# Optimization experiments

Measured on AMD Instinct MI355X. Metric: run time of the kernel, lower is better.

## Reference

```python
import jax, jax.numpy as jnp
import numpy as np

VOCAB = 50257
EMBED = 1024

def setup_inputs() -> dict:
    key = jax.random.key(0)
    k1, k2 = jax.random.split(key)
    hidden_states = jax.random.normal(k1, (2, 2048, EMBED), dtype=jnp.float32)
    # nn.Linear weight: [vocab_size, embed_dim], no bias
    W = jax.random.normal(k2, (VOCAB, EMBED), dtype=jnp.float32) * (1.0 / np.sqrt(EMBED))
    return {"hidden_states": hidden_states, "W": W}

def reference(hidden_states, W):
    # logits: [B, S, V] = hidden @ W^T
    logits = jnp.einsum("bsd,vd->bsv", hidden_states, W)
    return jax.nn.log_softmax(logits, axis=-1)
```

## Files before the change

### kernel.cpp

```cpp
#include <hip/hip_runtime.h>
#include <hip/hip_bf16.h>
#include <math.h>

#define VOCAB 50257
#define VPAD  50432
#define EMB   1024
#define NROWS 4096

#define BM 256
#define BN 256
#define BK 64
#define NKT (EMB / BK)
#define NMT (NROWS / BM)
#define NT  (VPAD / BN)
#define NWG (NMT * NT)

typedef __attribute__((ext_vector_type(4))) float  f32x4;
typedef __attribute__((ext_vector_type(4), aligned(4))) float f32x4u;
typedef __attribute__((ext_vector_type(4))) __bf16 bf16x4;
typedef __attribute__((ext_vector_type(8))) __bf16 bf16x8;

#define FENCE asm volatile("" ::: "memory")
#define BARRIER do { FENCE; __builtin_amdgcn_s_barrier(); FENCE; } while (0)

__global__ __launch_bounds__(256)
void cvt_bf16(const float* __restrict__ src, __bf16* __restrict__ dst,
              long n_src, long n_dst) {
    long i = ((long)blockIdx.x * 256 + threadIdx.x) * 8;
    if (i >= n_dst) return;
    bf16x8 o;
    if (i < n_src) {
        f32x4 a = *(const f32x4*)(src + i);
        f32x4 b = *(const f32x4*)(src + i + 4);
        #pragma unroll
        for (int e = 0; e < 4; ++e) {
            o[e]     = (__bf16)a[e];
            o[4 + e] = (__bf16)b[e];
        }
    } else {
        #pragma unroll
        for (int e = 0; e < 8; ++e) o[e] = (__bf16)0.0f;
    }
    *(bf16x8*)(dst + i) = o;
}

template <bool LB_OUT>
__global__ __launch_bounds__(512, 2)
void gemm_fused(const __bf16* __restrict__ A, const __bf16* __restrict__ B,
                float* __restrict__ C, __bf16* __restrict__ Lb,
                float* __restrict__ pbuf) {
    __shared__ alignas(16) __bf16 S[65536];

    const int tid  = threadIdx.x;
    const int lane = tid & 63;
    const int wave = tid >> 6;
    const int wm   = (wave >> 2) * 128;
    const int wn   = (wave & 3) * 64;
    const int frow = lane & 15;
    const int hi   = lane >> 4;

    const int b  = blockIdx.x;
    const int lg = (b & 7) * (NWG / 8) + (b >> 3);
    const int mt = lg & (NMT - 1);
    const int nt = lg >> 4;
    const int mtB = mt * BM, ntB = nt * BN;

    const int r0 = tid >> 3;
    const int ls = (tid & 7) ^ (r0 & 7);
    const __bf16* gA = A + (size_t)(mtB + r0) * EMB + ls * 8;
    const __bf16* gB = B + (size_t)(ntB + r0) * EMB + ls * 8;

    f32x4 acc[8][4];
    const f32x4 vzero = {0.f, 0.f, 0.f, 0.f};
    #pragma unroll
    for (int m = 0; m < 8; ++m)
        #pragma unroll
        for (int n = 0; n < 4; ++n) acc[m][n] = vzero;

#define STAGE_UNIT(bc, kt, u) do {                                            \
        const __bf16* g_ = ((u) < 2 ? gB : gA) + ((size_t)(((u)&1) * 128) * EMB + (kt) * BK); \
        __bf16* d_ = &S[(bc) * 32768 + ((u) < 2 ? 16384 : 0) + ((u)&1) * 8192 + wave * 512]; \
        __builtin_amdgcn_global_load_lds(                                     \
            (const __attribute__((address_space(1))) void*)g_,               \
            (__attribute__((address_space(3))) void*)d_, 16, 0, 0);          \
        __builtin_amdgcn_global_load_lds(                                     \
            (const __attribute__((address_space(1))) void*)(g_ + (size_t)64 * EMB), \
            (__attribute__((address_space(3))) void*)(d_ + 4096), 16, 0, 0); \
    } while (0)

#define LDA_F(c, mh, ks) { _Pragma("unroll")                                  \
    for (int i_ = 0; i_ < 4; ++i_) {                                          \
        const int row_ = wm + ((mh) * 4 + i_) * 16 + frow;                    \
        af[i_] = *(const bf16x8*)&S[(c) * 32768 + row_ * 64 + ((((ks) * 4 + hi)) ^ (row_ & 7)) * 8]; } }

#define LDB_F(c, ks) { _Pragma("unroll")                                      \
    for (int n_ = 0; n_ < 4; ++n_) {                                          \
        const int row_ = wn + n_ * 16 + frow;                                 \
        bfr[n_] = *(const bf16x8*)&S[(c) * 32768 + 16384 + row_ * 64 + ((((ks) * 4 + hi)) ^ (row_ & 7)) * 8]; } }

#define MFMA16(mh)                                                            \
    __builtin_amdgcn_s_setprio(1);                                            \
    _Pragma("unroll") for (int i_ = 0; i_ < 4; ++i_)                          \
        _Pragma("unroll") for (int n_ = 0; n_ < 4; ++n_)                      \
            acc[(mh) * 4 + i_][n_] = __builtin_amdgcn_mfma_f32_16x16x32_bf16( \
                af[i_], bfr[n_], acc[(mh) * 4 + i_][n_], 0, 0, 0);            \
    __builtin_amdgcn_s_setprio(0);

    bf16x8 af[4], bfr[4];

    #pragma unroll
    for (int u = 0; u < 4; ++u) STAGE_UNIT(0, 0, u);

    int cur = 0;
    for (int t = 0; t < NKT; ++t) {
        const int c = cur;
        const bool pf = (t + 1 < NKT);
        if (pf) {
            STAGE_UNIT(c ^ 1, t + 1, 0);
            asm volatile("s_waitcnt vmcnt(2)" ::: "memory");
        } else {
            asm volatile("s_waitcnt vmcnt(0)" ::: "memory");
        }
        BARRIER;
        LDB_F(c, 0); LDA_F(c, 0, 0); MFMA16(0);
        if (pf) STAGE_UNIT(c ^ 1, t + 1, 1);
        LDA_F(c, 1, 0); MFMA16(1);
        if (pf) STAGE_UNIT(c ^ 1, t + 1, 2);
        LDB_F(c, 1); LDA_F(c, 0, 1); MFMA16(0);
        if (pf) STAGE_UNIT(c ^ 1, t + 1, 3);
        LDA_F(c, 1, 1); MFMA16(1);
        BARRIER;
        cur ^= 1;
    }
#undef STAGE_UNIT

    __syncthreads();
    const bool edge = (ntB + BN > VOCAB);

    if (LB_OUT) {
        #pragma unroll
        for (int m = 0; m < 8; ++m) {
            const size_t rbase = (size_t)(mtB + wm + m * 16 + hi * 4) * VPAD;
            #pragma unroll
            for (int n = 0; n < 4; ++n) {
                const size_t col = ntB + wn + n * 16 + frow;
                #pragma unroll
                for (int r = 0; r < 4; ++r)
                    Lb[rbase + (size_t)r * VPAD + col] = (__bf16)acc[m][n][r];
            }
        }
    } else {
        #pragma unroll
        for (int m = 0; m < 8; ++m) {
            const size_t rbase = (size_t)(mtB + wm + m * 16 + hi * 4) * VOCAB;
            #pragma unroll
            for (int n = 0; n < 4; ++n) {
                const int col = ntB + wn + n * 16 + frow;
                if (!edge || col < VOCAB) {
                    #pragma unroll
                    for (int r = 0; r < 4; ++r)
                        C[rbase + (size_t)r * VOCAB + col] = acc[m][n][r];
                }
            }
        }
    }

    float* ldsP = (float*)&S[0];
    const int lcid = (wave & 3) * 16 + frow;
    #pragma unroll
    for (int m = 0; m < 8; ++m) {
        #pragma unroll
        for (int r = 0; r < 4; ++r) {
            float s = 0.0f;
            #pragma unroll
            for (int n = 0; n < 4; ++n) {
                if (!edge || (ntB + wn + n * 16 + frow) < VOCAB)
                    s += __expf(acc[m][n][r]);
            }
            ldsP[(wm + m * 16 + hi * 4 + r) * 68 + lcid] = s;
        }
    }
    __syncthreads();

    {
        const int rl = tid >> 1, hf = tid & 1;
        const float* q = ldsP + rl * 68 + hf * 32;
        float s = 0.0f;
        #pragma unroll
        for (int k = 0; k < 8; ++k) {
            f32x4 v = *(const f32x4*)(q + k * 4);
            s += v[0] + v[1] + v[2] + v[3];
        }
        s += __shfl_xor(s, 1);
        if (hf == 0) pbuf[(size_t)nt * NROWS + mtB + rl] = s;
    }
}

__global__ __launch_bounds__(256)
void lse_reduce(const float* __restrict__ pbuf, float* __restrict__ lse) {
    __shared__ float sl[4][64];
    const int r0 = blockIdx.x * 64;
    const int l  = threadIdx.x & 63;
    const int w  = threadIdx.x >> 6;
    float s = 0.0f;
    for (int t = w; t < NT; t += 4)
        s += pbuf[(size_t)t * NROWS + r0 + l];
    sl[w][l] = s;
    __syncthreads();
    if (threadIdx.x < 64)
        lse[r0 + l] = __logf(sl[0][l] + sl[1][l] + sl[2][l] + sl[3][l]);
}

__global__ __launch_bounds__(256)
void expand_sub(const __bf16* __restrict__ Lb, const float* __restrict__ lse,
                float* __restrict__ C) {
    const int row  = blockIdx.x >> 1;
    const int half = blockIdx.x & 1;
    const float s = lse[row];
    const __bf16* src = Lb + (size_t)row * VPAD;
    float* dst = C + (size_t)row * VOCAB;
    const int i0 = half * 3141;
    const int i1 = i0 + 3141;
    for (int i = i0 + threadIdx.x; i < i1; i += 256) {
        bf16x8 v = __builtin_nontemporal_load((const bf16x8*)(src + i * 8));
        f32x4u a, b2;
        a[0] = (float)v[0] - s; a[1] = (float)v[1] - s;
        a[2] = (float)v[2] - s; a[3] = (float)v[3] - s;
        b2[0] = (float)v[4] - s; b2[1] = (float)v[5] - s;
        b2[2] = (float)v[6] - s; b2[3] = (float)v[7] - s;
        __builtin_nontemporal_store(a,  (f32x4u*)(dst + i * 8));
        __builtin_nontemporal_store(b2, (f32x4u*)(dst + i * 8 + 4));
    }
    if (blockIdx.x == 0 && threadIdx.x == 0)
        C[50256] = (float)Lb[50256] - s;
    else if (half == 1 && threadIdx.x == 0)
        dst[50256] = (float)src[50256] - s;
}

__global__ __launch_bounds__(256)
void sub_lse(float* __restrict__ C, const float* __restrict__ lse) {
    const int row = blockIdx.x;
    const float s = lse[row];
    float* p = C + (size_t)row * VOCAB;
    for (int i = threadIdx.x; i < 12564; i += 256) {
        f32x4u v = *(const f32x4u*)(p + 4 * i);
        v[0] -= s; v[1] -= s; v[2] -= s; v[3] -= s;
        *(f32x4u*)(p + 4 * i) = v;
    }
    if (threadIdx.x == 0) p[50256] -= s;
}

#define FBM 128
#define FBK 32
__device__ __forceinline__ int swz_idx(int row, int col) {
    int slot = (col >> 3) ^ ((row >> 1) & 3);
    return row * FBK + slot * 8 + (col & 7);
}

__global__ __launch_bounds__(256, 2)
void gemm_logits(const float* __restrict__ H, const float* __restrict__ W,
                 float* __restrict__ C) {
    __shared__ __bf16 ldsA[FBM * FBK];
    __shared__ __bf16 ldsB[FBM * FBK];

    const int tid  = threadIdx.x;
    const int lane = tid & 63;
    const int wave = tid >> 6;
    const int wm = (wave >> 1) * 64;
    const int wn = (wave & 1) * 64;
    const int mt = blockIdx.x;
    const int nt = blockIdx.y;
    const int srow = tid >> 1;
    const int scol = (tid & 1) * 16;
    const int brow_g = nt * FBM + srow;
    const bool bvalid = brow_g < VOCAB;
    const float* aptr = H + (size_t)(mt * FBM + srow) * EMB + scol;
    const float* bptr = W + (size_t)(bvalid ? brow_g : 0) * EMB + scol;

    f32x4 areg[4], breg[4];
    #pragma unroll
    for (int q = 0; q < 4; ++q) {
        areg[q] = *(const f32x4*)(aptr + q * 4);
        breg[q] = *(const f32x4*)(bptr + q * 4);
    }
    f32x4 acc[4][4];
    const f32x4 vzero = {0.f, 0.f, 0.f, 0.f};
    #pragma unroll
    for (int i = 0; i < 4; ++i)
        #pragma unroll
        for (int j = 0; j < 4; ++j) acc[i][j] = vzero;

    const int frow = lane & 15;
    const int kcol = (lane >> 4) * 8;

    for (int kt = 0; kt < EMB / FBK; ++kt) {
        __syncthreads();
        #pragma unroll
        for (int q = 0; q < 4; ++q) {
            const int col = scol + q * 4;
            bf16x4 av, bv;
            #pragma unroll
            for (int e = 0; e < 4; ++e) {
                av[e] = (__bf16)areg[q][e];
                bv[e] = bvalid ? (__bf16)breg[q][e] : (__bf16)0.0f;
            }
            *(bf16x4*)(&ldsA[swz_idx(srow, col)]) = av;
            *(bf16x4*)(&ldsB[swz_idx(srow, col)]) = bv;
        }
        __syncthreads();
        if (kt + 1 < EMB / FBK) {
            const int ko = (kt + 1) * FBK;
            #pragma unroll
            for (int q = 0; q < 4; ++q) {
                areg[q] = *(const f32x4*)(aptr + ko + q * 4);
                breg[q] = *(const f32x4*)(bptr + ko + q * 4);
            }
        }
        bf16x8 af[4], bfr[4];
        #pragma unroll
        for (int i = 0; i < 4; ++i) {
            af[i]  = *(const bf16x8*)(&ldsA[swz_idx(wm + i * 16 + frow, kcol)]);
            bfr[i] = *(const bf16x8*)(&ldsB[swz_idx(wn + i * 16 + frow, kcol)]);
        }
        #pragma unroll
        for (int i = 0; i < 4; ++i)
            #pragma unroll
            for (int j = 0; j < 4; ++j)
                acc[i][j] = __builtin_amdgcn_mfma_f32_16x16x32_bf16(
                    af[i], bfr[j], acc[i][j], 0, 0, 0);
    }

    const int crow = mt * FBM + wm + (lane >> 4) * 4;
    const int ccol = nt * FBM + wn + (lane & 15);
    #pragma unroll
    for (int i = 0; i < 4; ++i) {
        #pragma unroll
        for (int j = 0; j < 4; ++j) {
            const int col = ccol + j * 16;
            if (col < VOCAB) {
                #pragma unroll
                for (int r = 0; r < 4; ++r)
                    C[(size_t)(crow + i * 16 + r) * VOCAB + col] = acc[i][j][r];
            }
        }
    }
}

__global__ __launch_bounds__(256)
void row_lse(const float* __restrict__ C, float* __restrict__ lse) {
    const int row = blockIdx.x;
    const float* p = C + (size_t)row * VOCAB;

    float m = -INFINITY, l = 0.0f;
    for (int i = threadIdx.x; i < 12564; i += 256) {
        f32x4u v = *(const f32x4u*)(p + 4 * i);
        #pragma unroll
        for (int e = 0; e < 4; ++e) {
            const float x  = v[e];
            const float mn = fmaxf(m, x);
            l = l * __expf(m - mn) + __expf(x - mn);
            m = mn;
        }
    }
    if (threadIdx.x == 0) {
        const float x  = p[50256];
        const float mn = fmaxf(m, x);
        l = l * __expf(m - mn) + __expf(x - mn);
        m = mn;
    }
    #pragma unroll
    for (int off = 1; off < 64; off <<= 1) {
        const float mo = __shfl_xor(m, off);
        const float lo = __shfl_xor(l, off);
        const float mn = fmaxf(m, mo);
        l = l * __expf(m - mn) + lo * __expf(mo - mn);
        m = mn;
    }
    __shared__ float sm[4], sl[4];
    if ((threadIdx.x & 63) == 0) { sm[threadIdx.x >> 6] = m; sl[threadIdx.x >> 6] = l; }
    __syncthreads();
    if (threadIdx.x == 0) {
        m = sm[0]; l = sl[0];
        #pragma unroll
        for (int w = 1; w < 4; ++w) {
            const float mn = fmaxf(m, sm[w]);
            l = l * __expf(m - mn) + sl[w] * __expf(sm[w] - mn);
            m = mn;
        }
        lse[row] = m + __logf(l);
    }
}

extern "C" void kernel_launch(void* const* d_in, const int* in_sizes, int n_in,
                              void* d_out, int out_size, void* d_ws, size_t ws_size,
                              hipStream_t stream) {
    const float* H = (const float*)d_in[0];
    const float* W = (const float*)d_in[1];
    float* C   = (float*)d_out;
    float* lse = (float*)d_ws;

    const long nH  = (long)NROWS * EMB;
    const long nW  = (long)VOCAB * EMB;
    const long nWp = (long)VPAD * EMB;

    const size_t pb_off   = 16384;
    const size_t pb_bytes = (size_t)NT * NROWS * sizeof(float);
    const size_t hb_off   = (pb_off + pb_bytes + 255) & ~(size_t)255;
    const size_t wb_off   = hb_off + (size_t)nH * 2;
    const size_t lb_off   = wb_off + (size_t)nWp * 2;
    const size_t lb_bytes = (size_t)NROWS * VPAD * 2;
    const size_t need_lb   = lb_off + lb_bytes;
    const size_t need_full = lb_off;

    if (ws_size >= need_full) {
        __bf16* Hb = (__bf16*)((char*)d_ws + hb_off);
        __bf16* Wb = (__bf16*)((char*)d_ws + wb_off);
        float*  pb = (float*)((char*)d_ws + pb_off);
        cvt_bf16<<<(int)(nH / 8 / 256), 256, 0, stream>>>(H, Hb, nH, nH);
        cvt_bf16<<<(int)((nWp / 8 + 255) / 256), 256, 0, stream>>>(W, Wb, nW, nWp);
        if (ws_size >= need_lb) {
            __bf16* Lb = (__bf16*)((char*)d_ws + lb_off);
            gemm_fused<true><<<dim3(NWG), 512, 0, stream>>>(Hb, Wb, C, Lb, pb);
            lse_reduce<<<dim3(NROWS / 64), 256, 0, stream>>>(pb, lse);
            expand_sub<<<dim3(NROWS * 2), 256, 0, stream>>>(Lb, lse, C);
        } else {
            gemm_fused<false><<<dim3(NWG), 512, 0, stream>>>(Hb, Wb, C, (__bf16*)nullptr, pb);
            lse_reduce<<<dim3(NROWS / 64), 256, 0, stream>>>(pb, lse);
            sub_lse<<<dim3(NROWS), 256, 0, stream>>>(C, lse);
        }
    } else {
        dim3 ggrid(NROWS / FBM, (VOCAB + FBM - 1) / FBM);
        gemm_logits<<<ggrid, 256, 0, stream>>>(H, W, C);
        row_lse<<<dim3(NROWS), 256, 0, stream>>>(C, lse);
        sub_lse<<<dim3(NROWS), 256, 0, stream>>>(C, lse);
    }
}
```

Before: 809.9 us.

## Restructure GEMM main loop into finer-grained staged LDS pipeline with split K-halves

Reorganizes the LDS layout so A is staged in per-M-half chunks and B in per-K-half chunks, each with its own swizzle. The K loop gets a deeper prefetch schedule that issues partial stages for tile t+1 and t+2 between MFMA groups, with barriers around each MFMA block. The aim is to hide global-to-LDS latency better and keep the matrix cores busy, at the cost of more barriers and more complex buffer reuse that risks races. It also removes a redundant extra write of the last element in the finalize kernel.

After: 823.2 us. No clear change (+1.6%).

```diff
diff --git a/kernel.cpp b/kernel.cpp
--- a/kernel.cpp
+++ b/kernel.cpp
@@ -65,11 +65,6 @@
     const int nt = lg >> 4;
     const int mtB = mt * BM, ntB = nt * BN;
 
-    const int r0 = tid >> 3;
-    const int ls = (tid & 7) ^ (r0 & 7);
-    const __bf16* gA = A + (size_t)(mtB + r0) * EMB + ls * 8;
-    const __bf16* gB = B + (size_t)(ntB + r0) * EMB + ls * 8;
-
     f32x4 acc[8][4];
     const f32x4 vzero = {0.f, 0.f, 0.f, 0.f};
     #pragma unroll
@@ -77,26 +72,46 @@
         #pragma unroll
         for (int n = 0; n < 4; ++n) acc[m][n] = vzero;
 
-#define STAGE_UNIT(bc, kt, u) do {                                            \
-        const __bf16* g_ = ((u) < 2 ? gB : gA) + ((size_t)(((u)&1) * 128) * EMB + (kt) * BK); \
-        __bf16* d_ = &S[(bc) * 32768 + ((u) < 2 ? 16384 : 0) + ((u)&1) * 8192 + wave * 512]; \
-        __builtin_amdgcn_global_load_lds(                                     \
-            (const __attribute__((address_space(1))) void*)g_,               \
-            (__attribute__((address_space(3))) void*)d_, 16, 0, 0);          \
-        __builtin_amdgcn_global_load_lds(                                     \
-            (const __attribute__((address_space(1))) void*)(g_ + (size_t)64 * EMB), \
-            (__attribute__((address_space(3))) void*)(d_ + 4096), 16, 0, 0); \
+#define GLOAD(gp, dp)                                                         \
+    __builtin_amdgcn_global_load_lds(                                         \
+        (const __attribute__((address_space(1))) void*)(gp),                 \
+        (__attribute__((address_space(3))) void*)(dp), 16, 0, 0)
+
+#define STAGE_A(bc, kt, mh) do {                                              \
+        int n_ = tid, lr_ = n_ >> 3;                                          \
+        int gr_ = (lr_ & 63) + (mh) * 64 + ((lr_ >> 6) << 7);                 \
+        GLOAD(A + (size_t)(mtB + gr_) * EMB + (kt) * BK                       \
+                + (((n_ & 7) ^ (lr_ & 7)) * 8),                               \
+              &S[(bc) * 32768 + (mh) * 8192 + wave * 512]);                   \
+        n_ = tid + 512; lr_ = n_ >> 3;                                        \
+        gr_ = (lr_ & 63) + (mh) * 64 + ((lr_ >> 6) << 7);                     \
+        GLOAD(A + (size_t)(mtB + gr_) * EMB + (kt) * BK                       \
+                + (((n_ & 7) ^ (lr_ & 7)) * 8),                               \
+              &S[(bc) * 32768 + (mh) * 8192 + 4096 + wave * 512]);            \
     } while (0)
 
-#define LDA_F(c, mh, ks) { _Pragma("unroll")                                  \
+#define STAGE_B(bc, kt, ks) do {                                              \
+        int n_ = tid, rb_ = n_ >> 2;                                          \
+        GLOAD(B + (size_t)(ntB + rb_) * EMB + (kt) * BK + (ks) * 32           \
+                + (((n_ & 3) ^ ((rb_ >> 1) & 3)) * 8),                        \
+              &S[(bc) * 32768 + 16384 + (ks) * 8192 + wave * 512]);           \
+        n_ = tid + 512; rb_ = n_ >> 2;                                        \
+        GLOAD(B + (size_t)(ntB + rb_) * EMB + (kt) * BK + (ks) * 32           \
+                + (((n_ & 3) ^ ((rb_ >> 1) & 3)) * 8),                        \
+              &S[(bc) * 32768 + 16384 + (ks) * 8192 + 4096 + wave * 512]);    \
+    } while (0)
+
+#define LDA_F(bc, mh, ks) { _Pragma("unroll")                                 \
     for (int i_ = 0; i_ < 4; ++i_) {                                          \
-        const int row_ = wm + ((mh) * 4 + i_) * 16 + frow;                    \
-        af[i_] = *(const bf16x8*)&S[(c) * 32768 + row_ * 64 + ((((ks) * 4 + hi)) ^ (row_ & 7)) * 8]; } }
-
-#define LDB_F(c, ks) { _Pragma("unroll")                                      \
+        const int lrow_ = (i_ * 16 + frow) + ((wm >> 7) << 6);                \
+        af[i_] = *(const bf16x8*)&S[(bc) * 32768 + (mh) * 8192               \
+            + lrow_ * 64 + ((((ks) * 4 + hi) ^ (lrow_ & 7)) * 8)]; } }
+
+#define LDB_F(bc, ks) { _Pragma("unroll")                                     \
     for (int n_ = 0; n_ < 4; ++n_) {                                          \
-        const int row_ = wn + n_ * 16 + frow;                                 \
-        bfr[n_] = *(const bf16x8*)&S[(c) * 32768 + 16384 + row_ * 64 + ((((ks) * 4 + hi)) ^ (row_ & 7)) * 8]; } }
+        const int rb_ = wn + n_ * 16 + frow;                                  \
+        bfr[n_] = *(const bf16x8*)&S[(bc) * 32768 + 16384 + (ks) * 8192      \
+            + rb_ * 32 + (((hi ^ ((rb_ >> 1) & 3))) * 8)]; } }
 
 #define MFMA16(mh)                                                            \
     __builtin_amdgcn_s_setprio(1);                                            \
@@ -108,31 +123,42 @@
 
     bf16x8 af[4], bfr[4];
 
-    #pragma unroll
-    for (int u = 0; u < 4; ++u) STAGE_UNIT(0, 0, u);
-
-    int cur = 0;
+    STAGE_B(0, 0, 0); STAGE_A(0, 0, 0); STAGE_B(0, 0, 1); STAGE_A(0, 0, 1);
+    STAGE_B(1, 1, 0); STAGE_A(1, 1, 0);
+    asm volatile("s_waitcnt vmcnt(4)" ::: "memory");
+    BARRIER;
+
     for (int t = 0; t < NKT; ++t) {
-        const int c = cur;
-        const bool pf = (t + 1 < NKT);
-        if (pf) {
-            STAGE_UNIT(c ^ 1, t + 1, 0);
-            asm volatile("s_waitcnt vmcnt(2)" ::: "memory");
-        } else {
-            asm volatile("s_waitcnt vmcnt(0)" ::: "memory");
-        }
-        BARRIER;
-        LDB_F(c, 0); LDA_F(c, 0, 0); MFMA16(0);
-        if (pf) STAGE_UNIT(c ^ 1, t + 1, 1);
-        LDA_F(c, 1, 0); MFMA16(1);
-        if (pf) STAGE_UNIT(c ^ 1, t + 1, 2);
-        LDB_F(c, 1); LDA_F(c, 0, 1); MFMA16(0);
-        if (pf) STAGE_UNIT(c ^ 1, t + 1, 3);
-        LDA_F(c, 1, 1); MFMA16(1);
-        BARRIER;
-        cur ^= 1;
-    }
-#undef STAGE_UNIT
+        const int c   = t & 1;
+        const bool p1 = (t + 1 < NKT);
+        const bool p2 = (t + 2 < NKT);
+
+        LDB_F(c, 0); LDA_F(c, 0, 0);
+        if (p1) STAGE_B(c ^ 1, t + 1, 1);
+        BARRIER;
+        MFMA16(0);
+        BARRIER;
+        LDA_F(c, 1, 0);
+        if (p1) STAGE_A(c ^ 1, t + 1, 1);
+        BARRIER;
+        MFMA16(1);
+        BARRIER;
+        LDB_F(c, 1); LDA_F(c, 0, 1);
+        if (p2) STAGE_B(c, t + 2, 0);
+        BARRIER;
+        MFMA16(0);
+        BARRIER;
+        LDA_F(c, 1, 1);
+        if (p2) STAGE_A(c, t + 2, 0);
+        if (p2)      asm volatile("s_waitcnt vmcnt(4)" ::: "memory");
+        else if (p1) asm volatile("s_waitcnt vmcnt(0)" ::: "memory");
+        BARRIER;
+        MFMA16(1);
+        BARRIER;
+    }
+#undef STAGE_A
+#undef STAGE_B
+#undef GLOAD
 
     __syncthreads();
     const bool edge = (ntB + BN > VOCAB);
@@ -231,9 +257,7 @@
         __builtin_nontemporal_store(a,  (f32x4u*)(dst + i * 8));
         __builtin_nontemporal_store(b2, (f32x4u*)(dst + i * 8 + 4));
     }
-    if (blockIdx.x == 0 && threadIdx.x == 0)
-        C[50256] = (float)Lb[50256] - s;
-    else if (half == 1 && threadIdx.x == 0)
+    if (half == 1 && threadIdx.x == 0)
         dst[50256] = (float)src[50256] - s;
 }
 
```
